# Kernel tuning notes

Measured on AMD Instinct MI355X. Metric: run time of the kernel, lower is better.

Reference implementation:

```python
import jax, jax.numpy as jnp
import numpy as np

B, S, L, F = 32, 48, 64, 256


def setup_inputs() -> dict:
    key = jax.random.key(0)
    ks = jax.random.split(key, 7)
    return {
        "features": jax.random.normal(ks[0], (B, S, L, F), dtype=jnp.float32),
        "src_locs": jax.random.normal(ks[1], (B, L, 2), dtype=jnp.float32),
        "tar_locs": jax.random.normal(ks[2], (B, 2), dtype=jnp.float32),
        "W1": jax.random.normal(ks[3], (F, F), dtype=jnp.float32) * (1.0 / np.sqrt(F)),
        "b1": jax.random.normal(ks[4], (F,), dtype=jnp.float32) * 0.02,
        "W2": jax.random.normal(ks[5], (F, 1), dtype=jnp.float32) * (1.0 / np.sqrt(F)),
        "b2": jax.random.normal(ks[6], (1,), dtype=jnp.float32) * 0.02,
    }


def reference(features, src_locs, tar_locs, W1, b1, W2, b2):
    # features: (B, S, L, F); src_locs: (B, L, 2); tar_locs: (B, 2)
    # MLP score: Linear(F,F) + ReLU + Linear(F,1) + ReLU -> (B, S, L, 1)
    attn = jax.nn.relu(jnp.einsum('bslf,fg->bslg', features, W1) + b1)
    attn = jax.nn.relu(jnp.einsum('bslf,fo->bslo', attn, W2) + b2)  # (B,S,L,1)
    # inverse-distance weights over stations: (B, L)
    dists = jnp.sqrt(jnp.sum((src_locs - tar_locs[:, None, :]) ** 2, axis=-1))
    inv_dists = 1.0 / dists  # (B, L)
    # broadcast to (B, 1, L, 1), softmax over src_length axis (axis=2)
    attn_scores = jax.nn.softmax(attn * inv_dists[:, None, :, None], axis=2)
    # weighted sum over stations -> (B, S, F)
    return jnp.sum(features * attn_scores, axis=2)
```

## Files before the change

### kernel.cpp

```cpp
#include <hip/hip_runtime.h>
#include <hip/hip_fp16.h>
#include <math.h>

typedef _Float16 half8 __attribute__((ext_vector_type(8)));
typedef _Float16 half4_t __attribute__((ext_vector_type(4)));
typedef float floatx4 __attribute__((ext_vector_type(4)));

#define BB 32
#define SS 48
#define LL 64
#define FF 256

#define WAVE_BARRIER() do {                                          \
    asm volatile("s_waitcnt lgkmcnt(0)" ::: "memory");               \
    __builtin_amdgcn_s_barrier();                                    \
    asm volatile("" ::: "memory");                                   \
} while (0)

#define ISSUE_FENCE() asm volatile("" ::: "memory")

__global__ __launch_bounds__(256) void prep_w(const float* __restrict__ W1,
                                              _Float16* __restrict__ whi,
                                              _Float16* __restrict__ wlo) {
    int idx = blockIdx.x * 256 + threadIdx.x;
    int j    = idx & 7;
    int lane = (idx >> 3) & 63;
    int nt   = (idx >> 9) & 15;
    int kt   = idx >> 13;
    int k = kt * 32 + ((lane >> 4) & 3) * 8 + j;
    int n = nt * 16 + (lane & 15);
    float x = W1[k * FF + n];
    _Float16 hi = (_Float16)x;
    _Float16 lo = (_Float16)(x - (float)hi);
    whi[idx] = hi;
    wlo[idx] = lo;
}

__global__ __launch_bounds__(512, 4) void ida_mfma(
    const float* __restrict__ features,
    const float* __restrict__ src_locs,
    const float* __restrict__ tar_locs,
    const _Float16* __restrict__ whi,
    const _Float16* __restrict__ wlo,
    const float* __restrict__ b1,
    const float* __restrict__ W2,
    const float* __restrict__ b2,
    float* __restrict__ out)
{
    __shared__ _Float16 Ahi[16384];
    __shared__ float SP[LL * 8];
    __shared__ float red[8 * FF];

    const int t    = threadIdx.x;
    const int w    = t >> 6;
    const int lane = t & 63;
    const int quad = lane >> 4;
    const int l16  = lane & 15;
    const int bs   = blockIdx.x;
    const int b    = bs / SS;

    const float* Xg = features + (size_t)bs * (LL * FF);

    float sx = src_locs[(b * LL + lane) * 2 + 0];
    float sy = src_locs[(b * LL + lane) * 2 + 1];
    float tx = tar_locs[b * 2 + 0];
    float ty = tar_locs[b * 2 + 1];
    float b2v = b2[0];
    float b1v[2], w2v[2];
    #pragma unroll
    for (int ntl = 0; ntl < 2; ++ntl) {
        int n = (w * 2 + ntl) * 16 + l16;
        b1v[ntl] = b1[n];
        w2v[ntl] = W2[n];
    }
    ISSUE_FENCE();

    float4 araw[8];
    #pragma unroll
    for (int it = 0; it < 4; ++it) {
        int G   = it * 8 + w;
        int row = (G >> 3) * 16 + l16;
        int cb  = (G & 7) * 32 + quad * 8;
        const float4* p = (const float4*)(Xg + row * FF + cb);
        araw[2 * it + 0] = p[0];
        araw[2 * it + 1] = p[1];
    }
    ISSUE_FENCE();

    half8 bh[2], bl[2], nbh[2], nbl[2];
    #pragma unroll
    for (int ntl = 0; ntl < 2; ++ntl) {
        size_t off = ((size_t)(0 * 16 + (w * 2 + ntl)) * 64 + lane) * 8;
        bh[ntl] = *((const half8*)(whi + off));
        bl[ntl] = *((const half8*)(wlo + off));
    }
    ISSUE_FENCE();

    #pragma unroll
    for (int it = 0; it < 4; ++it) {
        int G = it * 8 + w;
        float4 x0 = araw[2 * it + 0], x1 = araw[2 * it + 1];
        float xs[8] = {x0.x, x0.y, x0.z, x0.w, x1.x, x1.y, x1.z, x1.w};
        half8 hi;
        #pragma unroll
        for (int j = 0; j < 8; ++j) hi[j] = (_Float16)xs[j];
        *((half8*)&Ahi[(G * 64 + lane) * 8]) = hi;
    }

    WAVE_BARRIER();

    floatx4 acc[4][2] = {};

    #pragma unroll
    for (int kt = 0; kt < 8; ++kt) {
        if (kt < 7) {
            #pragma unroll
            for (int ntl = 0; ntl < 2; ++ntl) {
                size_t off = ((size_t)((kt + 1) * 16 + (w * 2 + ntl)) * 64 + lane) * 8;
                nbh[ntl] = *((const half8*)(whi + off));
                nbl[ntl] = *((const half8*)(wlo + off));
            }
        }
        #pragma unroll
        for (int mt = 0; mt < 4; ++mt) {
            half8 ahi = *((half8*)&Ahi[((mt * 8 + kt) * 64 + lane) * 8]);
            #pragma unroll
            for (int ntl = 0; ntl < 2; ++ntl) {
                acc[mt][ntl] = __builtin_amdgcn_mfma_f32_16x16x32_f16(ahi, bh[ntl], acc[mt][ntl], 0, 0, 0);
                acc[mt][ntl] = __builtin_amdgcn_mfma_f32_16x16x32_f16(ahi, bl[ntl], acc[mt][ntl], 0, 0, 0);
            }
        }
        if (kt < 7) {
            bh[0] = nbh[0]; bh[1] = nbh[1];
            bl[0] = nbl[0]; bl[1] = nbl[1];
        }
    }

    #pragma unroll
    for (int mt = 0; mt < 4; ++mt) {
        #pragma unroll
        for (int r = 0; r < 4; ++r) {
            float p = 0.f;
            #pragma unroll
            for (int ntl = 0; ntl < 2; ++ntl) {
                float h = fmaxf(acc[mt][ntl][r] + b1v[ntl], 0.f);
                p = fmaf(h, w2v[ntl], p);
            }
            p += __shfl_xor(p, 1);
            p += __shfl_xor(p, 2);
            p += __shfl_xor(p, 4);
            p += __shfl_xor(p, 8);
            if (l16 == 0) SP[(mt * 16 + quad * 4 + r) * 8 + w] = p;
        }
    }

    WAVE_BARRIER();

    float s = SP[8 * lane + 0] + SP[8 * lane + 1] + SP[8 * lane + 2] + SP[8 * lane + 3]
            + SP[8 * lane + 4] + SP[8 * lane + 5] + SP[8 * lane + 6] + SP[8 * lane + 7] + b2v;
    float score = fmaxf(s, 0.f);
    float dxv = sx - tx, dyv = sy - ty;
    float inv_d = 1.0f / sqrtf(dxv * dxv + dyv * dyv);
    float logit = score * inv_d;
    float m = logit;
    #pragma unroll
    for (int o = 32; o > 0; o >>= 1) m = fmaxf(m, __shfl_xor(m, o));
    float e = __expf(logit - m);
    float se = e;
    #pragma unroll
    for (int o = 32; o > 0; o >>= 1) se += __shfl_xor(se, o);
    float wgt = e / se;

    {
        floatx4 o4 = {0.f, 0.f, 0.f, 0.f};
        #pragma unroll
        for (int lr = 0; lr < 8; ++lr) {
            int r  = w * 8 + lr;
            float wl = __shfl(wgt, r);
            int G2 = (r >> 4) * 8 + (lane >> 3);
            int ei = (G2 * 64 + ((lane >> 1) & 3) * 16 + (r & 15)) * 8 + (lane & 1) * 4;
            half4_t hv = *((const half4_t*)&Ahi[ei]);
            o4[0] = fmaf((float)hv[0], wl, o4[0]);
            o4[1] = fmaf((float)hv[1], wl, o4[1]);
            o4[2] = fmaf((float)hv[2], wl, o4[2]);
            o4[3] = fmaf((float)hv[3], wl, o4[3]);
        }
        *((floatx4*)&red[w * FF + lane * 4]) = o4;
    }

    WAVE_BARRIER();

    if (t < FF) {
        float o = red[0 * FF + t] + red[1 * FF + t] + red[2 * FF + t] + red[3 * FF + t]
                + red[4 * FF + t] + red[5 * FF + t] + red[6 * FF + t] + red[7 * FF + t];
        out[(size_t)bs * FF + t] = o;
    }
}

extern "C" void kernel_launch(void* const* d_in, const int* in_sizes, int n_in,
                              void* d_out, int out_size, void* d_ws, size_t ws_size,
                              hipStream_t stream) {
    const float* features = (const float*)d_in[0];
    const float* src_locs = (const float*)d_in[1];
    const float* tar_locs = (const float*)d_in[2];
    const float* W1       = (const float*)d_in[3];
    const float* b1       = (const float*)d_in[4];
    const float* W2       = (const float*)d_in[5];
    const float* b2       = (const float*)d_in[6];
    float* out = (float*)d_out;

    _Float16* whi = (_Float16*)d_ws;
    _Float16* wlo = whi + FF * FF;

    prep_w<<<dim3(FF * FF / 256), dim3(256), 0, stream>>>(W1, whi, wlo);
    ida_mfma<<<dim3(BB * SS), dim3(512), 0, stream>>>(
        features, src_locs, tar_locs, whi, wlo, b1, W2, b2, out);
}
```

Baseline: 182.7 us.

## Drop W1 hi/lo split, raise occupancy, reduce output via shuffles

Removes the low-order fp16 residual of W1, so the GEMM runs one MFMA per tile instead of two and loads half the weight data. The weighted feature sum is now done with in-register FMAs and cross-lane shuffle reductions, which drops the 8 KB shared reduction buffer and a barrier. The launch bound's waves-per-EU hint is raised from 4 to 6. The cost is lower precision in the MLP scores, since W1 is now carried in fp16 only, and added register pressure from the eight shuffle accumulators.

```diff
diff --git a/kernel.cpp b/kernel.cpp
--- a/kernel.cpp
+++ b/kernel.cpp
@@ -3,7 +3,6 @@
 #include <math.h>
 
 typedef _Float16 half8 __attribute__((ext_vector_type(8)));
-typedef _Float16 half4_t __attribute__((ext_vector_type(4)));
 typedef float floatx4 __attribute__((ext_vector_type(4)));
 
 #define BB 32
@@ -20,8 +19,7 @@
 #define ISSUE_FENCE() asm volatile("" ::: "memory")
 
 __global__ __launch_bounds__(256) void prep_w(const float* __restrict__ W1,
-                                              _Float16* __restrict__ whi,
-                                              _Float16* __restrict__ wlo) {
+                                              _Float16* __restrict__ whi) {
     int idx = blockIdx.x * 256 + threadIdx.x;
     int j    = idx & 7;
     int lane = (idx >> 3) & 63;
@@ -29,19 +27,14 @@
     int kt   = idx >> 13;
     int k = kt * 32 + ((lane >> 4) & 3) * 8 + j;
     int n = nt * 16 + (lane & 15);
-    float x = W1[k * FF + n];
-    _Float16 hi = (_Float16)x;
-    _Float16 lo = (_Float16)(x - (float)hi);
-    whi[idx] = hi;
-    wlo[idx] = lo;
+    whi[idx] = (_Float16)W1[k * FF + n];
 }
 
-__global__ __launch_bounds__(512, 4) void ida_mfma(
+__global__ __launch_bounds__(512, 6) void ida_mfma(
     const float* __restrict__ features,
     const float* __restrict__ src_locs,
     const float* __restrict__ tar_locs,
     const _Float16* __restrict__ whi,
-    const _Float16* __restrict__ wlo,
     const float* __restrict__ b1,
     const float* __restrict__ W2,
     const float* __restrict__ b2,
@@ -49,7 +42,6 @@
 {
     __shared__ _Float16 Ahi[16384];
     __shared__ float SP[LL * 8];
-    __shared__ float red[8 * FF];
 
     const int t    = threadIdx.x;
     const int w    = t >> 6;
@@ -87,12 +79,11 @@
     }
     ISSUE_FENCE();
 
-    half8 bh[2], bl[2], nbh[2], nbl[2];
+    half8 bh[2], nbh[2];
     #pragma unroll
     for (int ntl = 0; ntl < 2; ++ntl) {
         size_t off = ((size_t)(0 * 16 + (w * 2 + ntl)) * 64 + lane) * 8;
         bh[ntl] = *((const half8*)(whi + off));
-        bl[ntl] = *((const half8*)(wlo + off));
     }
     ISSUE_FENCE();
 
@@ -118,22 +109,16 @@
             for (int ntl = 0; ntl < 2; ++ntl) {
                 size_t off = ((size_t)((kt + 1) * 16 + (w * 2 + ntl)) * 64 + lane) * 8;
                 nbh[ntl] = *((const half8*)(whi + off));
-                nbl[ntl] = *((const half8*)(wlo + off));
             }
         }
         #pragma unroll
         for (int mt = 0; mt < 4; ++mt) {
             half8 ahi = *((half8*)&Ahi[((mt * 8 + kt) * 64 + lane) * 8]);
             #pragma unroll
-            for (int ntl = 0; ntl < 2; ++ntl) {
+            for (int ntl = 0; ntl < 2; ++ntl)
                 acc[mt][ntl] = __builtin_amdgcn_mfma_f32_16x16x32_f16(ahi, bh[ntl], acc[mt][ntl], 0, 0, 0);
-                acc[mt][ntl] = __builtin_amdgcn_mfma_f32_16x16x32_f16(ahi, bl[ntl], acc[mt][ntl], 0, 0, 0);
-            }
         }
-        if (kt < 7) {
-            bh[0] = nbh[0]; bh[1] = nbh[1];
-            bl[0] = nbl[0]; bl[1] = nbl[1];
-        }
+        if (kt < 7) { bh[0] = nbh[0]; bh[1] = nbh[1]; }
     }
 
     #pragma unroll
@@ -171,29 +156,27 @@
     for (int o = 32; o > 0; o >>= 1) se += __shfl_xor(se, o);
     float wgt = e / se;
 
-    {
-        floatx4 o4 = {0.f, 0.f, 0.f, 0.f};
-        #pragma unroll
-        for (int lr = 0; lr < 8; ++lr) {
-            int r  = w * 8 + lr;
-            float wl = __shfl(wgt, r);
-            int G2 = (r >> 4) * 8 + (lane >> 3);
-            int ei = (G2 * 64 + ((lane >> 1) & 3) * 16 + (r & 15)) * 8 + (lane & 1) * 4;
-            half4_t hv = *((const half4_t*)&Ahi[ei]);
-            o4[0] = fmaf((float)hv[0], wl, o4[0]);
-            o4[1] = fmaf((float)hv[1], wl, o4[1]);
-            o4[2] = fmaf((float)hv[2], wl, o4[2]);
-            o4[3] = fmaf((float)hv[3], wl, o4[3]);
-        }
-        *((floatx4*)&red[w * FF + lane * 4]) = o4;
-    }
-
-    WAVE_BARRIER();
-
-    if (t < FF) {
-        float o = red[0 * FF + t] + red[1 * FF + t] + red[2 * FF + t] + red[3 * FF + t]
-                + red[4 * FF + t] + red[5 * FF + t] + red[6 * FF + t] + red[7 * FF + t];
-        out[(size_t)bs * FF + t] = o;
+    float o8[8] = {0.f, 0.f, 0.f, 0.f, 0.f, 0.f, 0.f, 0.f};
+    #pragma unroll
+    for (int it = 0; it < 4; ++it) {
+        float wr = __shfl(wgt, it * 16 + l16);
+        half8 hv = *((half8*)&Ahi[((it * 8 + w) * 64 + lane) * 8]);
+        #pragma unroll
+        for (int j = 0; j < 8; ++j)
+            o8[j] = fmaf((float)hv[j], wr, o8[j]);
+    }
+    #pragma unroll
+    for (int o = 1; o < 16; o <<= 1) {
+        #pragma unroll
+        for (int j = 0; j < 8; ++j)
+            o8[j] += __shfl_xor(o8[j], o);
+    }
+    if (l16 == 0) {
+        float* op = out + (size_t)bs * FF + w * 32 + quad * 8;
+        float4 s0 = {o8[0], o8[1], o8[2], o8[3]};
+        float4 s1 = {o8[4], o8[5], o8[6], o8[7]};
+        *((float4*)op) = s0;
+        *((float4*)(op + 4)) = s1;
     }
 }
 
@@ -210,9 +193,8 @@
     float* out = (float*)d_out;
 
     _Float16* whi = (_Float16*)d_ws;
-    _Float16* wlo = whi + FF * FF;
-
-    prep_w<<<dim3(FF * FF / 256), dim3(256), 0, stream>>>(W1, whi, wlo);
+
+    prep_w<<<dim3(FF * FF / 256), dim3(256), 0, stream>>>(W1, whi);
     ida_mfma<<<dim3(BB * SS), dim3(512), 0, stream>>>(
-        features, src_locs, tar_locs, whi, wlo, b1, W2, b2, out);
+        features, src_locs, tar_locs, whi, b1, W2, b2, out);
 }
```

After: 176.1 us. 3.6% less time.
